# Performance work log

Measured on AMD Instinct MI355X. Metric: run time of the kernel, lower is better.

Reference implementation:

```python
import jax, jax.numpy as jnp
import numpy as np

B, S, D, H = 64, 197, 1024, 4096

# I-BERT IntGELU constants: erf(x) ~ a*(x+b)^2 + c on [0,-b], integer-only form
K_SQRT2 = 1.4142          # sqrt(2)
GELU_SHIFT = 14           # 2**14 right-shift to avoid accumulator overflow
COEF_A = -0.2888
COEF_B = -1.769
COEF_C = 1.0 / COEF_A     # c folded by a, as in I-BERT (coeff[2] /= coeff[0])


def setup_inputs() -> dict:
    key = jax.random.key(0)
    k1, k2, k3, k4, k5, k6 = jax.random.split(key, 6)
    x_int = jax.random.randint(k1, (B, S, D), 0, 127).astype(jnp.int32)  # int8-range activations
    s_x = jax.random.uniform(k2, (1,), jnp.float32, 0.01, 0.03)          # per-tensor act scale
    w1 = jax.random.normal(k3, (H, D), jnp.float32) * 0.02
    b1 = jax.random.normal(k4, (H,), jnp.float32) * 0.02
    w2 = jax.random.normal(k5, (D, H), jnp.float32) * 0.02
    b2 = jax.random.normal(k6, (D,), jnp.float32) * 0.02
    return {"x_int": x_int, "s_x": s_x, "w1": w1, "b1": b1, "w2": w2, "b2": b2}


def _quant_weight(w):
    # per-tensor symmetric int8 weight quantization (QuantLinearWithWeight)
    s_w = jnp.max(jnp.abs(w)) / 127.0
    w_int = jnp.clip(jnp.round(w / s_w), -127.0, 127.0)
    return w_int, s_w


def _quant_linear(x_int, s_x, w, b):
    # integer GEMM: int8 acts x int8 weights -> int32 accumulator, scale s_x*s_w
    w_int, s_w = _quant_weight(w)
    s_out = s_x * s_w
    b_int = jnp.round(b / s_out)  # bias quantized into the accumulator scale
    acc = jnp.einsum('bsd,hd->bsh', x_int, w_int) + b_int
    return acc, s_out


def _int_erf(x_int, sf):
    # integer polynomial approx of erf (I-BERT)
    b_int = jnp.floor(COEF_B / sf)
    c_int = jnp.floor(COEF_C / sf ** 2)
    sign = jnp.sign(x_int)
    abs_int = jnp.minimum(jnp.abs(x_int), -b_int)
    y_int = sign * ((abs_int + b_int) ** 2 + c_int)
    sf_out = sf ** 2 * COEF_A
    y_int = jnp.floor(y_int / 2.0 ** GELU_SHIFT)  # shift to keep accumulator in range
    return y_int, sf_out * 2.0 ** GELU_SHIFT


def _int_gelu(x_int, sf):
    # GELU(x) = x * 0.5 * (1 + erf(x/sqrt(2))), integer-only
    sig_int, sig_sf = _int_erf(x_int, sf / K_SQRT2)
    shift_int = jnp.floor(1.0 / sig_sf)  # torch: 1.0 // sigmoid_scaling_factor
    y_int = x_int * (sig_int + shift_int)
    return y_int, sf * sig_sf / 2.0


def _quant_act(x_int, sf):
    # QuantAct: requantize int32-scale activations back to int8 (dynamic per-tensor scale)
    x_hat = x_int * sf
    s_a = jnp.max(jnp.abs(x_hat)) / 127.0
    q = jnp.clip(jnp.round(x_hat / s_a), -128.0, 127.0)
    return q, s_a


def reference(x_int, s_x, w1, b1, w2, b2):
    x = x_int.astype(jnp.float32)
    s = s_x[0]
    x, s = _quant_linear(x, s, w1, b1)   # [B,S,H] int32 accumulator
    x, s = _int_gelu(x, s)               # integer-only GELU
    x, s = _quant_act(x, s)              # requant -> int8 range
    # dropout_1 is identity in eval mode
    x, s = _quant_linear(x, s, w2, b2)   # [B,S,D] int32 accumulator
    # dropout_2 is identity in eval mode
    return x, s
```

## Files before the change

kernel.cpp:

```cpp
#include <hip/hip_runtime.h>
#include <cstdint>
#include <cstddef>

constexpr int Bb = 64, Ss = 197, Dd = 1024, Hh = 4096;
constexpr int M  = Bb * Ss;
constexpr int MT = (M + 127) / 128;
constexpr int Mpad = MT * 128;
constexpr int NBLK1 = (Hh / 128) * MT;

#define SL_S1    4
#define SL_BERF  5
#define SL_CERF  6
#define SL_SHIFT 7
#define SL_S2    8
#define SL_SA    9
#define SL_SOUT2 10
#define SL_SW1   11
#define SL_SW2   12

typedef int v4i __attribute__((ext_vector_type(4)));

#define GLD_LDS(g, l) \
  __builtin_amdgcn_global_load_lds((const __attribute__((address_space(1))) void*)(g), \
                                   (__attribute__((address_space(3))) void*)(l), 16, 0, 0)

__device__ __forceinline__ float blockmax256(float m) {
  #pragma unroll
  for (int off = 32; off; off >>= 1) m = fmaxf(m, __shfl_down(m, off, 64));
  __shared__ float wm[4];
  int lane = threadIdx.x & 63, wid = threadIdx.x >> 6;
  if (lane == 0) wm[wid] = m;
  __syncthreads();
  return fmaxf(fmaxf(wm[0], wm[1]), fmaxf(wm[2], wm[3]));
}

__global__ void k_wmax(const float* __restrict__ w1, const float* __restrict__ w2,
                       int n4, float* __restrict__ pmax) {
  int b = blockIdx.x;
  const float4* s4 = (const float4*)(b < 512 ? w1 : w2);
  float m = 0.f;
  for (int i = (b & 511) * 256 + threadIdx.x; i < n4; i += 512 * 256) {
    float4 v = s4[i];
    m = fmaxf(m, fmaxf(fmaxf(fabsf(v.x), fabsf(v.y)), fmaxf(fabsf(v.z), fabsf(v.w))));
  }
  m = blockmax256(m);
  if (threadIdx.x == 0) pmax[b] = m;
}

__global__ void k_scalars1(unsigned* slu, const float* __restrict__ pmax,
                           const float* __restrict__ s_x_ptr) {
  int t = threadIdx.x;
  float m1 = fmaxf(pmax[t], pmax[t + 256]);
  float m2 = fmaxf(pmax[512 + t], pmax[768 + t]);
  __shared__ float r1[256], r2[256];
  r1[t] = m1; r2[t] = m2;
  __syncthreads();
  for (int s = 128; s; s >>= 1) {
    if (t < s) { r1[t] = fmaxf(r1[t], r1[t + s]); r2[t] = fmaxf(r2[t], r2[t + s]); }
    __syncthreads();
  }
  if (t == 0) {
    float* slf = (float*)slu;
    float s_w1 = r1[0] / 127.0f;
    float s_w2 = r2[0] / 127.0f;
    float s1  = s_x_ptr[0] * s_w1;
    float sfe = s1 / 1.4142f;
    float berf = floorf(-1.769f / sfe);
    float cerf = floorf(((float)(1.0 / -0.2888)) / (sfe * sfe));
    float sig  = ((sfe * sfe) * -0.2888f) * 16384.0f;
    float shiftv = floorf(1.0f / sig);
    float s2 = (s1 * sig) / 2.0f;
    slf[SL_S1] = s1; slf[SL_BERF] = berf; slf[SL_CERF] = cerf;
    slf[SL_SHIFT] = shiftv; slf[SL_S2] = s2; slf[SL_SW1] = s_w1; slf[SL_SW2] = s_w2;
  }
}

__global__ void k_scalars2(unsigned* slu, const float* __restrict__ pmax,
                           float* dout_scalar) {
  int t = threadIdx.x;
  float m = 0.f;
  for (int i = t; i < NBLK1; i += 256) m = fmaxf(m, pmax[i]);
  __shared__ float r1[256];
  r1[t] = m;
  __syncthreads();
  for (int s = 128; s; s >>= 1) {
    if (t < s) r1[t] = fmaxf(r1[t], r1[t + s]);
    __syncthreads();
  }
  if (t == 0) {
    float* slf = (float*)slu;
    float xm = fabsf(r1[0] * slf[SL_S2]);
    float sa = xm / 127.0f;
    float sout2 = sa * slf[SL_SW2];
    slf[SL_SA] = sa; slf[SL_SOUT2] = sout2;
    *dout_scalar = sout2;
  }
}

__global__ void k_quantcvt(const float* __restrict__ w1, const float* __restrict__ w2,
                           const int* __restrict__ x, const unsigned* __restrict__ slu,
                           int8_t* __restrict__ w1q, int8_t* __restrict__ w2q,
                           int8_t* __restrict__ xq) {
  const float* slf = (const float*)slu;
  float sw1 = slf[SL_SW1], sw2 = slf[SL_SW2];
  const int n1 = Hh * Dd / 4, n2 = Dd * Hh / 4;
  const int nx = M * Dd / 4, n3 = Mpad * Dd / 4;
  const int total = n1 + n2 + n3;
  for (int i = blockIdx.x * blockDim.x + threadIdx.x; i < total; i += gridDim.x * blockDim.x) {
    if (i < n1 + n2) {
      bool first = i < n1;
      int idx = first ? i : i - n1;
      float sw = first ? sw1 : sw2;
      float4 v = ((const float4*)(first ? w1 : w2))[idx];
      int qa = (int)fminf(fmaxf(rintf(v.x / sw), -127.f), 127.f);
      int qb = (int)fminf(fmaxf(rintf(v.y / sw), -127.f), 127.f);
      int qc = (int)fminf(fmaxf(rintf(v.z / sw), -127.f), 127.f);
      int qd = (int)fminf(fmaxf(rintf(v.w / sw), -127.f), 127.f);
      unsigned p = (unsigned)(qa & 0xff) | ((unsigned)(qb & 0xff) << 8) |
                   ((unsigned)(qc & 0xff) << 16) | ((unsigned)(qd & 0xff) << 24);
      ((unsigned*)(first ? w1q : w2q))[idx] = p;
    } else {
      int idx = i - n1 - n2;
      unsigned p = 0u;
      if (idx < nx) {
        int4 v = ((const int4*)x)[idx];
        p = (unsigned)(v.x & 0xff) | ((unsigned)(v.y & 0xff) << 8) |
            ((unsigned)(v.z & 0xff) << 16) | ((unsigned)(v.w & 0xff) << 24);
      }
      ((unsigned*)xq)[idx] = p;
    }
  }
}

__global__ __launch_bounds__(256) void k_requant(const float* __restrict__ y,
                                                 const unsigned* __restrict__ slu,
                                                 int8_t* __restrict__ q) {
  const float* slf = (const float*)slu;
  float r_req = slf[SL_S2] / slf[SL_SA];
  const int n16 = M * Hh / 16;
  for (int i = blockIdx.x * blockDim.x + threadIdx.x; i < n16; i += gridDim.x * blockDim.x) {
    const float4* yp = (const float4*)y + (size_t)i * 4;
    unsigned pk[4];
    #pragma unroll
    for (int v = 0; v < 4; v++) {
      float4 t = yp[v];
      int a = (int)fminf(fmaxf(rintf(t.x * r_req), -128.f), 127.f);
      int b = (int)fminf(fmaxf(rintf(t.y * r_req), -128.f), 127.f);
      int c = (int)fminf(fmaxf(rintf(t.z * r_req), -128.f), 127.f);
      int d = (int)fminf(fmaxf(rintf(t.w * r_req), -128.f), 127.f);
      pk[v] = (unsigned)(a & 0xff) | ((unsigned)(b & 0xff) << 8) |
              ((unsigned)(c & 0xff) << 16) | ((unsigned)(d & 0xff) << 24);
    }
    *(v4i*)(q + (size_t)i * 16) = *(const v4i*)pk;
  }
}

template <int K, int MODE, int GMAP>
__global__ __launch_bounds__(256) void k_gemm(
    const int8_t* __restrict__ A, const int8_t* __restrict__ Bm,
    const float* __restrict__ bias, const unsigned* __restrict__ slu,
    int8_t* __restrict__ qout, float* __restrict__ fout, float* __restrict__ pmax_y,
    int Mreal, int Ncols) {
  __shared__ alignas(16) int8_t smem[32768];
  int8_t* As = smem;
  int8_t* Bs = smem + 16384;
  const int t = threadIdx.x;
  const int d = blockIdx.x;
  int bm, bn;
  if constexpr (GMAP == 0) {
    int xcd = d & 7, slot = d >> 3;
    bm = slot >> 2;
    bn = xcd * 4 + (slot & 3);
  } else {
    bn = d & 7;
    bm = d >> 3;
  }
  const int lane = t & 63, wid = t >> 6;
  const int wRow = (wid >> 1) * 64, wCol = (wid & 1) * 64;
  const int lm = lane & 15, quad = lane >> 4;

  v4i acc[4][4] = {};

  const size_t aBase = (size_t)bm * 128 * K;
  const size_t bBase = (size_t)bn * 128 * K;

  for (int k0 = 0; k0 < K; k0 += 128) {
    #pragma unroll
    for (int c = 0; c < 4; c++) {
      int s = c * 256 + t;
      int row = s >> 3;
      int cb = (s & 7) ^ (row & 7);
      size_t goff = (size_t)row * K + k0 + cb * 16;
      GLD_LDS(A + aBase + goff, As + s * 16);
      GLD_LDS(Bm + bBase + goff, Bs + s * 16);
    }
    __syncthreads();
    #pragma unroll
    for (int ks = 0; ks < 2; ks++) {
      v4i af[4], bf[4];
      #pragma unroll
      for (int i = 0; i < 4; i++) {
        int r = wRow + i * 16 + lm;
        af[i] = *(const v4i*)(As + r * 128 + (((ks * 4 + quad) ^ (r & 7)) << 4));
      }
      #pragma unroll
      for (int i = 0; i < 4; i++) {
        int r = wCol + i * 16 + lm;
        bf[i] = *(const v4i*)(Bs + r * 128 + (((ks * 4 + quad) ^ (r & 7)) << 4));
      }
      #pragma unroll
      for (int i = 0; i < 4; i++)
        #pragma unroll
        for (int j = 0; j < 4; j++)
          acc[i][j] = __builtin_amdgcn_mfma_i32_16x16x64_i8(bf[j], af[i], acc[i][j], 0, 0, 0);
    }
    __syncthreads();
  }

  const float* slf = (const float*)slu;
  if constexpr (MODE == 2) {
    float sout2 = slf[SL_SOUT2];
    float4 bq[4];
    #pragma unroll
    for (int j = 0; j < 4; j++) {
      float4 bv = *(const float4*)(bias + bn * 128 + wCol + j * 16 + quad * 4);
      bq[j].x = rintf(bv.x / sout2); bq[j].y = rintf(bv.y / sout2);
      bq[j].z = rintf(bv.z / sout2); bq[j].w = rintf(bv.w / sout2);
    }
    #pragma unroll
    for (int i = 0; i < 4; i++) {
      int gr = bm * 128 + wRow + i * 16 + lm;
      if (gr < Mreal) {
        #pragma unroll
        for (int j = 0; j < 4; j++) {
          int gc0 = bn * 128 + wCol + j * 16 + quad * 4;
          float4 o;
          o.x = (float)acc[i][j][0] + bq[j].x;
          o.y = (float)acc[i][j][1] + bq[j].y;
          o.z = (float)acc[i][j][2] + bq[j].z;
          o.w = (float)acc[i][j][3] + bq[j].w;
          *(float4*)(fout + (size_t)gr * Ncols + gc0) = o;
        }
      }
    }
  } else {
    float s1 = slf[SL_S1], berf = slf[SL_BERF], cerf = slf[SL_CERF], shiftv = slf[SL_SHIFT];
    float s2 = slf[SL_S2];
    float sa = (MODE == 1) ? slf[SL_SA] : 1.0f;
    float r_req = (MODE == 1) ? (s2 / sa) : 1.0f;
    float lmax = 0.f;
    float4 bq[4];
    #pragma unroll
    for (int j = 0; j < 4; j++) {
      float4 bv = *(const float4*)(bias + bn * 128 + wCol + j * 16 + quad * 4);
      bq[j].x = rintf(bv.x / s1); bq[j].y = rintf(bv.y / s1);
      bq[j].z = rintf(bv.z / s1); bq[j].w = rintf(bv.w / s1);
    }
    #pragma unroll
    for (int i = 0; i < 4; i++) {
      int mrow = wRow + i * 16 + lm;
      int gr = bm * 128 + mrow;
      bool rowok = gr < Mreal;
      #pragma unroll
      for (int j = 0; j < 4; j++) {
        int n0 = wCol + j * 16 + quad * 4;
        unsigned packed = 0u;
        float4 y4;
        #pragma unroll
        for (int r = 0; r < 4; r++) {
          float a = (float)acc[i][j][r] + ((const float*)&bq[j])[r];
          float ax = fminf(fabsf(a), -berf);
          float tt = ax + berf;
          float u = tt * tt + cerf;
          float ye = (a < 0.f) ? -u : u;
          float yv = floorf(ye * (1.0f / 16384.0f));
          float y = a * (yv + shiftv);
          if constexpr (MODE == 0) {
            if (rowok) lmax = fmaxf(lmax, fabsf(y));
          } else if constexpr (MODE == 3) {
            if (rowok) lmax = fmaxf(lmax, fabsf(y));
            ((float*)&y4)[r] = y;
          } else {
            float qf = rintf(y * r_req);
            qf = fminf(fmaxf(qf, -128.f), 127.f);
            packed |= ((unsigned)((int)qf & 0xff)) << (8 * r);
          }
        }
        if constexpr (MODE == 1) {
          *(unsigned*)(smem + mrow * 132 + n0) = packed;
        }
        if constexpr (MODE == 3) {
          if (rowok) *(float4*)(fout + (size_t)gr * Ncols + bn * 128 + n0) = y4;
        }
      }
    }
    if constexpr (MODE == 0 || MODE == 3) {
      #pragma unroll
      for (int off = 32; off; off >>= 1) lmax = fmaxf(lmax, __shfl_down(lmax, off, 64));
      float* red = (float*)smem;
      if (lane == 0) red[wid] = lmax;
      __syncthreads();
      if (t == 0) {
        float b = fmaxf(fmaxf(red[0], red[1]), fmaxf(red[2], red[3]));
        pmax_y[d] = b;
      }
    } else {
      __syncthreads();
      #pragma unroll
      for (int c2 = 0; c2 < 4; c2++) {
        int idx = c2 * 256 + t;
        int row = idx >> 3, c16 = (idx & 7) << 4;
        v4i v = *(const v4i*)(smem + row * 132 + c16);
        *(v4i*)(qout + (size_t)(bm * 128 + row) * Ncols + bn * 128 + c16) = v;
      }
    }
  }
}

extern "C" void kernel_launch(void* const* d_in, const int* in_sizes, int n_in,
                              void* d_out, int out_size, void* d_ws, size_t ws_size,
                              hipStream_t stream) {
  const int*   x   = (const int*)d_in[0];
  const float* s_x = (const float*)d_in[1];
  const float* w1  = (const float*)d_in[2];
  const float* b1  = (const float*)d_in[3];
  const float* w2  = (const float*)d_in[4];
  const float* b2  = (const float*)d_in[5];
  float* out = (float*)d_out;

  char* ws = (char*)d_ws;
  unsigned* slots = (unsigned*)ws;
  float* pmax_w = (float*)(ws + 1024);
  float* pmax_y = (float*)(ws + 8192);
  int8_t* w1q = (int8_t*)(ws + 32768);
  int8_t* w2q = w1q + (size_t)Hh * Dd;
  int8_t* xq  = w2q + (size_t)Dd * Hh;
  int8_t* qbuf = xq + (size_t)Mpad * Dd;
  float*  ybuf = (float*)(qbuf + (size_t)Mpad * Hh);

  size_t need = 32768 + 2 * (size_t)Hh * Dd + (size_t)Mpad * Dd
              + (size_t)Mpad * Hh + (size_t)M * Hh * 4;

  k_wmax<<<1024, 256, 0, stream>>>(w1, w2, Hh * Dd / 4, pmax_w);
  k_scalars1<<<1, 256, 0, stream>>>(slots, pmax_w, s_x);
  k_quantcvt<<<1024, 256, 0, stream>>>(w1, w2, x, slots, w1q, w2q, xq);

  if (ws_size >= need) {
    k_gemm<Dd, 3, 0><<<NBLK1, 256, 0, stream>>>(xq, w1q, b1, slots, nullptr, ybuf,
                                                pmax_y, M, Hh);
    k_scalars2<<<1, 256, 0, stream>>>(slots, pmax_y, out + (size_t)M * Dd);
    k_requant<<<2048, 256, 0, stream>>>(ybuf, slots, qbuf);
  } else {
    k_gemm<Dd, 0, 0><<<NBLK1, 256, 0, stream>>>(xq, w1q, b1, slots, nullptr, nullptr,
                                                pmax_y, M, Hh);
    k_scalars2<<<1, 256, 0, stream>>>(slots, pmax_y, out + (size_t)M * Dd);
    k_gemm<Dd, 1, 0><<<NBLK1, 256, 0, stream>>>(xq, w1q, b1, slots, qbuf, nullptr,
                                                nullptr, M, Hh);
  }
  k_gemm<Hh, 2, 1><<<8 * MT, 256, 0, stream>>>(qbuf, w2q, b2, slots, nullptr, out,
                                               nullptr, M, Dd);
}
```

Measured before the change: 385.7 us.

## Load GEMM MFMA fragments directly from global memory, bypassing LDS staging

The int8 GEMM no longer stages 128x128 A/B tiles in LDS through global_load_lds with barriers. Each wave now loads its MFMA operand fragments straight from global memory into registers and double-buffers them across the two k-halves. This removes the LDS round trip and the __syncthreads. In exchange, every operand is fetched redundantly by the two waves that share it, the global accesses are strided 16-byte reads per lane, and register pressure rises.

```diff
diff --git a/kernel.cpp b/kernel.cpp
--- a/kernel.cpp
+++ b/kernel.cpp
@@ -19,10 +19,6 @@
 #define SL_SW2   12
 
 typedef int v4i __attribute__((ext_vector_type(4)));
-
-#define GLD_LDS(g, l) \
-  __builtin_amdgcn_global_load_lds((const __attribute__((address_space(1))) void*)(g), \
-                                   (__attribute__((address_space(3))) void*)(l), 16, 0, 0)
 
 __device__ __forceinline__ float blockmax256(float m) {
   #pragma unroll
@@ -162,8 +158,6 @@
     int8_t* __restrict__ qout, float* __restrict__ fout, float* __restrict__ pmax_y,
     int Mreal, int Ncols) {
   __shared__ alignas(16) int8_t smem[32768];
-  int8_t* As = smem;
-  int8_t* Bs = smem + 16384;
   const int t = threadIdx.x;
   const int d = blockIdx.x;
   int bm, bn;
@@ -181,40 +175,42 @@
 
   v4i acc[4][4] = {};
 
-  const size_t aBase = (size_t)bm * 128 * K;
-  const size_t bBase = (size_t)bn * 128 * K;
-
+  const int8_t* pa[4];
+  const int8_t* pb[4];
+  #pragma unroll
+  for (int i = 0; i < 4; i++) {
+    pa[i] = A  + (size_t)(bm * 128 + wRow + i * 16 + lm) * K + quad * 16;
+    pb[i] = Bm + (size_t)(bn * 128 + wCol + i * 16 + lm) * K + quad * 16;
+  }
+
+  v4i a0[4], b0[4], a1[4], b1[4];
+  #pragma unroll
+  for (int i = 0; i < 4; i++) { a0[i] = *(const v4i*)(pa[i]); b0[i] = *(const v4i*)(pb[i]); }
+
+  #pragma unroll 1
   for (int k0 = 0; k0 < K; k0 += 128) {
     #pragma unroll
-    for (int c = 0; c < 4; c++) {
-      int s = c * 256 + t;
-      int row = s >> 3;
-      int cb = (s & 7) ^ (row & 7);
-      size_t goff = (size_t)row * K + k0 + cb * 16;
-      GLD_LDS(A + aBase + goff, As + s * 16);
-      GLD_LDS(Bm + bBase + goff, Bs + s * 16);
-    }
-    __syncthreads();
-    #pragma unroll
-    for (int ks = 0; ks < 2; ks++) {
-      v4i af[4], bf[4];
+    for (int i = 0; i < 4; i++) {
+      a1[i] = *(const v4i*)(pa[i] + k0 + 64);
+      b1[i] = *(const v4i*)(pb[i] + k0 + 64);
+    }
+    #pragma unroll
+    for (int i = 0; i < 4; i++)
+      #pragma unroll
+      for (int j = 0; j < 4; j++)
+        acc[i][j] = __builtin_amdgcn_mfma_i32_16x16x64_i8(b0[j], a0[i], acc[i][j], 0, 0, 0);
+    if (k0 + 128 < K) {
       #pragma unroll
       for (int i = 0; i < 4; i++) {
-        int r = wRow + i * 16 + lm;
-        af[i] = *(const v4i*)(As + r * 128 + (((ks * 4 + quad) ^ (r & 7)) << 4));
-      }
-      #pragma unroll
-      for (int i = 0; i < 4; i++) {
-        int r = wCol + i * 16 + lm;
-        bf[i] = *(const v4i*)(Bs + r * 128 + (((ks * 4 + quad) ^ (r & 7)) << 4));
-      }
-      #pragma unroll
-      for (int i = 0; i < 4; i++)
-        #pragma unroll
-        for (int j = 0; j < 4; j++)
-          acc[i][j] = __builtin_amdgcn_mfma_i32_16x16x64_i8(bf[j], af[i], acc[i][j], 0, 0, 0);
-    }
-    __syncthreads();
+        a0[i] = *(const v4i*)(pa[i] + k0 + 128);
+        b0[i] = *(const v4i*)(pb[i] + k0 + 128);
+      }
+    }
+    #pragma unroll
+    for (int i = 0; i < 4; i++)
+      #pragma unroll
+      for (int j = 0; j < 4; j++)
+        acc[i][j] = __builtin_amdgcn_mfma_i32_16x16x64_i8(b1[j], a1[i], acc[i][j], 0, 0, 0);
   }
 
   const float* slf = (const float*)slu;
```

Measured after the change: 756.9 us. 1.96x slower.
